# Performance work log

Hardware: AMD Instinct MI355X
Metric: run time of the kernel (lower is better)

The kernel has to match this reference:

```python
import jax, jax.numpy as jnp
import numpy as np

B, T, D = 2, 2048, 2048
H, KV = 16, 4
HD = D // H  # 128
ROPE_BASE = 10000.0


def _rope(t):
    # t: [B, h, T, HD]; faithful to torch apply_rope (even/odd split, concat halves)
    pos = jnp.arange(T, dtype=t.dtype)
    inv_freq = 1.0 / (ROPE_BASE ** (jnp.arange(0, HD, 2, dtype=t.dtype) / HD))
    ang = jnp.einsum('t,f->tf', pos, inv_freq)  # [T, HD/2]
    sin = jnp.sin(ang)[None, None]
    cos = jnp.cos(ang)[None, None]
    t1, t2 = t[..., ::2], t[..., 1::2]
    return jnp.concatenate([t1 * cos - t2 * sin, t1 * sin + t2 * cos], axis=-1)


def setup_inputs() -> dict:
    key = jax.random.key(0)
    kx, kq, kk, kv, ko = jax.random.split(key, 5)
    x = jax.random.normal(kx, (B, T, D), dtype=jnp.float32)
    s = 0.02
    Wq = jax.random.normal(kq, (D, D), dtype=jnp.float32) * s
    Wk = jax.random.normal(kk, (D, KV * HD), dtype=jnp.float32) * s
    Wv = jax.random.normal(kv, (D, KV * HD), dtype=jnp.float32) * s
    Wo = jax.random.normal(ko, (D, D), dtype=jnp.float32) * s
    return {"x": x, "Wq": Wq, "Wk": Wk, "Wv": Wv, "Wo": Wo}


def reference(x, Wq, Wk, Wv, Wo):
    # projections (nn.Linear, no bias)
    q = (x @ Wq).reshape(B, T, H, HD).transpose(0, 2, 1, 3)    # [B,H,T,HD]
    k = (x @ Wk).reshape(B, T, KV, HD).transpose(0, 2, 1, 3)   # [B,KV,T,HD]
    v = (x @ Wv).reshape(B, T, KV, HD).transpose(0, 2, 1, 3)
    q = _rope(q)
    k = _rope(k)
    # GQA: repeat_interleave kv heads to full head count
    g = H // KV
    k = jnp.repeat(k, g, axis=1)
    v = jnp.repeat(v, g, axis=1)
    # causal SDPA, default scale 1/sqrt(head_dim)
    scale = 1.0 / jnp.sqrt(jnp.array(HD, dtype=x.dtype))
    scores = jnp.einsum('bhqd,bhkd->bhqk', q, k) * scale
    mask = jnp.tril(jnp.ones((T, T), dtype=bool))
    scores = jnp.where(mask, scores, jnp.finfo(scores.dtype).min)
    attn = jax.nn.softmax(scores, axis=-1)
    out = jnp.einsum('bhqk,bhkd->bhqd', attn, v)               # [B,H,T,HD]
    out = out.transpose(0, 2, 1, 3).reshape(B, T, D)
    return out @ Wo
```

## Files before the change

### kernel.cpp

```cpp
#include <hip/hip_runtime.h>
#include <math.h>

#define BB 2
#define TT 2048
#define DD 2048
#define HH 16
#define KVHN 4
#define HDIM 128
#define NKV 3072

typedef unsigned short u16;
typedef unsigned int u32;
typedef __bf16 bf16x8 __attribute__((ext_vector_type(8)));
typedef float  f32x4  __attribute__((ext_vector_type(4)));

#define AS1 __attribute__((address_space(1)))
#define AS3 __attribute__((address_space(3)))

__device__ __forceinline__ void dma16(const u16* g, u16* l) {
  __builtin_amdgcn_global_load_lds((const AS1 u32*)g, (AS3 u32*)l, 16, 0, 0);
}

__device__ __forceinline__ u16 f2bf(float f) {
  u32 u = __float_as_uint(f);
  u32 r = (u + 0x7FFFu + ((u >> 16) & 1u)) >> 16;
  return (u16)r;
}
__device__ __forceinline__ float bf2f(u32 h) { return __uint_as_float(h << 16); }

__device__ __forceinline__ u32 pack2(float a, float b) {
  union { __bf16 h[2]; u32 u; } cv;
  cv.h[0] = (__bf16)a; cv.h[1] = (__bf16)b;
  return cv.u;
}

__global__ __launch_bounds__(256) void castf2b(const float* __restrict__ in,
                                               u16* __restrict__ out) {
  size_t i4 = (size_t)blockIdx.x * 256 + threadIdx.x;
  float4 v = *(const float4*)(in + i4 * 4);
  ushort4 o;
  o.x = f2bf(v.x); o.y = f2bf(v.y); o.z = f2bf(v.z); o.w = f2bf(v.w);
  *(ushort4*)(out + i4 * 4) = o;
}

__global__ __launch_bounds__(256) void tcast(const float* __restrict__ W,
                                             u16* __restrict__ WT,
                                             int K, int N) {
  __shared__ float tile[32][33];
  const int n0 = blockIdx.x * 32, k0 = blockIdx.y * 32;
  const int r = threadIdx.x >> 3;
  const int c4 = (threadIdx.x & 7) * 4;
  float4 v = *(const float4*)(W + (size_t)(k0 + r) * N + n0 + c4);
  tile[r][c4 + 0] = v.x; tile[r][c4 + 1] = v.y;
  tile[r][c4 + 2] = v.z; tile[r][c4 + 3] = v.w;
  __syncthreads();
  ushort4 o;
  o.x = f2bf(tile[c4 + 0][r]); o.y = f2bf(tile[c4 + 1][r]);
  o.z = f2bf(tile[c4 + 2][r]); o.w = f2bf(tile[c4 + 3][r]);
  *(ushort4*)(WT + (size_t)(n0 + r) * K + k0 + c4) = o;
}

template <int OUT_BF16>
__global__ __launch_bounds__(256) void gemm2(const u16* __restrict__ A,
                                             const u16* __restrict__ BT,
                                             void* __restrict__ Cv,
                                             int N, int K) {
  __shared__ u16 As[128 * 32];
  __shared__ u16 Bs[128 * 32];
  const int t = threadIdx.x;
  const int l = t & 63, w = t >> 6;
  const int lm = l & 15, quad = l >> 4;
  const int wm = w & 1, wn = w >> 1;
  const int m0 = blockIdx.y * 128, n0 = blockIdx.x * 128;
  const int wu = __builtin_amdgcn_readfirstlane(w);

  f32x4 acc[4][4];
  #pragma unroll
  for (int i = 0; i < 4; ++i)
    #pragma unroll
    for (int j = 0; j < 4; ++j) acc[i][j] = (f32x4){0.f, 0.f, 0.f, 0.f};

  for (int k0 = 0; k0 < K; k0 += 32) {
    __syncthreads();
    #pragma unroll
    for (int i = 0; i < 2; ++i) {
      int p0 = (wu * 2 + i) * 64;
      int p = p0 + l;
      int row = p >> 2, c = p & 3;
      dma16(A  + (size_t)(m0 + row) * K + k0 + c * 8, &As[p0 * 8]);
      dma16(BT + (size_t)(n0 + row) * K + k0 + c * 8, &Bs[p0 * 8]);
    }
    __syncthreads();
    bf16x8 a[4], bq[4];
    #pragma unroll
    for (int i = 0; i < 4; ++i)
      a[i] = *(const bf16x8*)&As[(wm * 64 + i * 16 + lm) * 32 + quad * 8];
    #pragma unroll
    for (int j = 0; j < 4; ++j)
      bq[j] = *(const bf16x8*)&Bs[(wn * 64 + j * 16 + lm) * 32 + quad * 8];
    #pragma unroll
    for (int i = 0; i < 4; ++i)
      #pragma unroll
      for (int j = 0; j < 4; ++j)
        acc[i][j] = __builtin_amdgcn_mfma_f32_16x16x32_bf16(a[i], bq[j], acc[i][j], 0, 0, 0);
  }

  #pragma unroll
  for (int i = 0; i < 4; ++i) {
    #pragma unroll
    for (int r = 0; r < 4; ++r) {
      size_t gr = (size_t)(m0 + wm * 64 + i * 16 + quad * 4 + r);
      #pragma unroll
      for (int j = 0; j < 4; ++j) {
        int gc = n0 + wn * 64 + j * 16 + lm;
        if (OUT_BF16) ((u16*)Cv)[gr * N + gc] = f2bf(acc[i][j][r]);
        else          ((float*)Cv)[gr * N + gc] = acc[i][j][r];
      }
    }
  }
}

__global__ __launch_bounds__(256) void rope2(u16* p) {
  const int row = blockIdx.x;
  const int pos = row & (TT - 1);
  u16* base = p + (size_t)row * NKV;
  float e0[5], e1[5];
  #pragma unroll
  for (int i = 0; i < 5; ++i) {
    int item = threadIdx.x + i * 256;
    int h20 = item >> 6, f = item & 63;
    int col = (h20 < 16) ? h20 * 128 : 2048 + (h20 - 16) * 128;
    u32 u = *(const u32*)(base + col + 2 * f);
    e0[i] = bf2f(u & 0xffffu);
    e1[i] = bf2f(u >> 16);
  }
  __syncthreads();
  #pragma unroll
  for (int i = 0; i < 5; ++i) {
    int item = threadIdx.x + i * 256;
    int h20 = item >> 6, f = item & 63;
    int col = (h20 < 16) ? h20 * 128 : 2048 + (h20 - 16) * 128;
    float sc = (h20 < 16) ? 0.08838834764831845f : 1.0f;
    float inv = exp2f((float)f * -0.20762050593046898f);
    float ang = (float)pos * inv;
    float sn = sinf(ang), cs = cosf(ang);
    base[col + f]      = f2bf((e0[i] * cs - e1[i] * sn) * sc);
    base[col + 64 + f] = f2bf((e0[i] * sn + e1[i] * cs) * sc);
  }
}

__global__ __launch_bounds__(256) void vtrans(const u16* __restrict__ QKV,
                                              u16* __restrict__ Vt) {
  __shared__ u16 tl[64][72];
  const int t0 = blockIdx.x * 64;
  const int y  = blockIdx.y;
  const int b  = blockIdx.z;
  #pragma unroll
  for (int i = 0; i < 2; ++i) {
    int idx = threadIdx.x + i * 256;
    int r = idx >> 3, c = (idx & 7) * 8;
    *(uint4*)&tl[r][c] =
        *(const uint4*)(QKV + (size_t)(b * TT + t0 + r) * NKV + 2560 + y * 64 + c);
  }
  __syncthreads();
  const int vh = y >> 1;
  #pragma unroll
  for (int i = 0; i < 2; ++i) {
    int idx = threadIdx.x + i * 256;
    int dr = idx >> 3, tc = (idx & 7) * 8;
    u16 tmp[8];
    #pragma unroll
    for (int j = 0; j < 8; ++j) tmp[j] = tl[tc + j][dr];
    int dloc = (y & 1) * 64 + dr;
    *(uint4*)(Vt + (size_t)((b * KVHN + vh) * HDIM + dloc) * TT + t0 + tc) =
        *(const uint4*)tmp;
  }
}

__global__ __launch_bounds__(256, 2) void attn2(const u16* __restrict__ QKV,
                                                const u16* __restrict__ Vt,
                                                u16* __restrict__ Ob) {
  __shared__ u16 KsA[64 * 128], KsB[64 * 128];
  __shared__ u16 VsA[128 * 64], VsB[128 * 64];
  __shared__ u16 Pw[4 * 2048];
  const int t = threadIdx.x;
  const int l = t & 63, w = t >> 6;
  const int lm = l & 15, quad = l >> 4;
  const int px = blockIdx.x, h = blockIdx.y, b = blockIdx.z;
  const int kvh = h >> 2;
  const int qlo = px * 64, qhi = (31 - px) * 64;
  const int last = 31 - px;
  const int wu = __builtin_amdgcn_readfirstlane(w);
  u16* pwv = &Pw[w * 2048];
  constexpr float L2E = 1.4426950408889634f;

  bf16x8 qf[2][4];
  {
    size_t r0 = (size_t)(b * TT + qlo + w * 16 + lm) * NKV + h * HDIM;
    size_t r1 = (size_t)(b * TT + qhi + w * 16 + lm) * NKV + h * HDIM;
    #pragma unroll
    for (int ks = 0; ks < 4; ++ks) {
      qf[0][ks] = *(const bf16x8*)(QKV + r0 + ks * 32 + quad * 8);
      qf[1][ks] = *(const bf16x8*)(QKV + r1 + ks * 32 + quad * 8);
    }
  }

  f32x4 o[8][2];
  #pragma unroll
  for (int i = 0; i < 8; ++i)
    #pragma unroll
    for (int n = 0; n < 2; ++n) o[i][n] = (f32x4){0.f, 0.f, 0.f, 0.f};
  float m_[2] = {-1e30f, -1e30f}, l_[2] = {0.f, 0.f};

  auto stageK = [&](int kt, u16* dst) {
    #pragma unroll
    for (int i = 0; i < 4; ++i) {
      int p0 = (wu * 4 + i) * 64;
      int p = p0 + l;
      int row = p >> 4, cp = p & 15, cl = cp ^ (row & 15);
      dma16(QKV + (size_t)(b * TT + kt * 64 + row) * NKV + 2048 + kvh * HDIM + cl * 8,
            dst + p0 * 8);
    }
  };
  auto stageV = [&](int kt, u16* dst) {
    #pragma unroll
    for (int i = 0; i < 4; ++i) {
      int p0 = (wu * 4 + i) * 64;
      int p = p0 + l;
      int d = p >> 3, cp = p & 7, cl = cp ^ (d & 7);
      dma16(Vt + (size_t)((b * KVHN + kvh) * HDIM + d) * TT + kt * 64 + cl * 8,
            dst + p0 * 8);
    }
  };

  auto body = [&](int kt, u16* kcur, u16* vcur, u16* knext, u16* vnext) {
    __syncthreads();
    const bool pf = kt < last;
    if (pf) stageV(kt + 1, vnext);
    const bool lo = (kt <= px);

    f32x4 s[4][2];
    #pragma unroll
    for (int mt = 0; mt < 4; ++mt) {
      s[mt][0] = (f32x4){0.f, 0.f, 0.f, 0.f};
      s[mt][1] = (f32x4){0.f, 0.f, 0.f, 0.f};
    }
    #pragma unroll
    for (int ks = 0; ks < 4; ++ks) {
      #pragma unroll
      for (int mt = 0; mt < 4; ++mt) {
        bf16x8 kb = *(const bf16x8*)&kcur[(mt * 16 + lm) * 128 + (((ks * 4 + quad) ^ lm) * 8)];
        if (lo) s[mt][0] = __builtin_amdgcn_mfma_f32_16x16x32_bf16(kb, qf[0][ks], s[mt][0], 0, 0, 0);
        s[mt][1] = __builtin_amdgcn_mfma_f32_16x16x32_bf16(kb, qf[1][ks], s[mt][1], 0, 0, 0);
      }
    }
    if (pf) stageK(kt + 1, knext);

    if (kt == px) {
      #pragma unroll
      for (int mt = 0; mt < 4; ++mt)
        #pragma unroll
        for (int r = 0; r < 4; ++r) {
          int kv = kt * 64 + mt * 16 + quad * 4 + r;
          if (kv > qlo + w * 16 + lm) s[mt][0][r] = -1e30f;
        }
    }
    if (kt == last) {
      #pragma unroll
      for (int mt = 0; mt < 4; ++mt)
        #pragma unroll
        for (int r = 0; r < 4; ++r) {
          int kv = kt * 64 + mt * 16 + quad * 4 + r;
          if (kv > qhi + w * 16 + lm) s[mt][1][r] = -1e30f;
        }
    }

    float al[2] = {1.f, 1.f};
    #pragma unroll
    for (int nt = 0; nt < 2; ++nt) {
      if (nt == 0 && !lo) continue;
      float mx = -1e30f;
      #pragma unroll
      for (int mt = 0; mt < 4; ++mt)
        #pragma unroll
        for (int r = 0; r < 4; ++r) mx = fmaxf(mx, s[mt][nt][r]);
      mx = fmaxf(mx, __shfl_xor(mx, 16));
      mx = fmaxf(mx, __shfl_xor(mx, 32));
      float mn = fmaxf(m_[nt], mx);
      al[nt] = exp2f((m_[nt] - mn) * L2E);
      m_[nt] = mn;
      float sum = 0.f;
      #pragma unroll
      for (int mt = 0; mt < 4; ++mt)
        #pragma unroll
        for (int r = 0; r < 4; ++r) {
          float pv = exp2f((s[mt][nt][r] - mn) * L2E);
          s[mt][nt][r] = pv;
          sum += pv;
        }
      sum += __shfl_xor(sum, 16);
      sum += __shfl_xor(sum, 32);
      l_[nt] = l_[nt] * al[nt] + sum;

      #pragma unroll
      for (int mt = 0; mt < 4; ++mt) {
        u32 p01 = pack2(s[mt][nt][0], s[mt][nt][1]);
        u32 p23 = pack2(s[mt][nt][2], s[mt][nt][3]);
        int phys = (mt * 2 + (quad >> 1)) ^ (lm & 7);
        int addr = (nt * 16 + lm) * 64 + phys * 8 + (quad & 1) * 4;
        uint2 uv; uv.x = p01; uv.y = p23;
        *(uint2*)&pwv[addr] = uv;
      }
      if (__any(al[nt] < 1.0f)) {
        #pragma unroll
        for (int mt2 = 0; mt2 < 8; ++mt2)
          #pragma unroll
          for (int r = 0; r < 4; ++r) o[mt2][nt][r] *= al[nt];
      }
    }

    #pragma unroll
    for (int ks2 = 0; ks2 < 2; ++ks2) {
      int coff = ((ks2 * 4 + quad) ^ (lm & 7)) * 8;
      bf16x8 pb0, pb1;
      if (lo) pb0 = *(const bf16x8*)&pwv[lm * 64 + coff];
      pb1 = *(const bf16x8*)&pwv[(16 + lm) * 64 + coff];
      #pragma unroll
      for (int mt2 = 0; mt2 < 8; ++mt2) {
        bf16x8 vb = *(const bf16x8*)&vcur[(mt2 * 16 + lm) * 64 + coff];
        if (lo) o[mt2][0] = __builtin_amdgcn_mfma_f32_16x16x32_bf16(vb, pb0, o[mt2][0], 0, 0, 0);
        o[mt2][1] = __builtin_amdgcn_mfma_f32_16x16x32_bf16(vb, pb1, o[mt2][1], 0, 0, 0);
      }
    }
  };

  stageK(0, KsA); stageV(0, VsA);
  for (int kt = 0; kt <= last; ++kt) {
    if ((kt & 1) == 0) body(kt, KsA, VsA, KsB, VsB);
    else               body(kt, KsB, VsB, KsA, VsA);
  }

  #pragma unroll
  for (int nt = 0; nt < 2; ++nt) {
    float inv = 1.f / l_[nt];
    #pragma unroll
    for (int mt2 = 0; mt2 < 8; ++mt2) {
      u32 a0 = pack2(o[mt2][nt][0] * inv, o[mt2][nt][1] * inv);
      u32 a1 = pack2(o[mt2][nt][2] * inv, o[mt2][nt][3] * inv);
      int phys = (mt2 * 2 + (quad >> 1)) ^ (lm & 7);
      int addr = lm * 128 + phys * 8 + (quad & 1) * 4;
      uint2 uv; uv.x = a0; uv.y = a1;
      *(uint2*)&pwv[addr] = uv;
    }
    int qt0 = nt ? qhi : qlo;
    #pragma unroll
    for (int i = 0; i < 4; ++i) {
      int p = i * 64 + l;
      int row = p >> 4, cl = p & 15;
      int cph = cl ^ (row & 7);
      uint4 val = *(const uint4*)&pwv[row * 128 + cph * 8];
      *(uint4*)(Ob + (size_t)(b * TT + qt0 + w * 16 + row) * DD + h * HDIM + cl * 8) = val;
    }
  }
}

extern "C" void kernel_launch(void* const* d_in, const int* in_sizes, int n_in,
                              void* d_out, int out_size, void* d_ws, size_t ws_size,
                              hipStream_t stream) {
  const float* x  = (const float*)d_in[0];
  const float* Wq = (const float*)d_in[1];
  const float* Wk = (const float*)d_in[2];
  const float* Wv = (const float*)d_in[3];
  const float* Wo = (const float*)d_in[4];
  float* out = (float*)d_out;

  u16* xb    = (u16*)d_ws;
  u16* WqkvT = xb + 8388608;
  u16* WoT   = xb + 14680064;
  u16* Vt    = WqkvT;
  u16* Ob    = xb;
  u16* QKVb  = (u16*)d_out;

  dim3 blk(256);
  castf2b<<<8192, blk, 0, stream>>>(x, xb);
  tcast<<<dim3(64, 64), blk, 0, stream>>>(Wq, WqkvT, DD, DD);
  tcast<<<dim3(16, 64), blk, 0, stream>>>(Wk, WqkvT + (size_t)2048 * DD, DD, 512);
  tcast<<<dim3(16, 64), blk, 0, stream>>>(Wv, WqkvT + (size_t)2560 * DD, DD, 512);
  tcast<<<dim3(64, 64), blk, 0, stream>>>(Wo, WoT, DD, DD);

  gemm2<1><<<dim3(NKV / 128, 32), blk, 0, stream>>>(xb, WqkvT, QKVb, NKV, DD);
  rope2<<<BB * TT, blk, 0, stream>>>(QKVb);
  vtrans<<<dim3(32, 8, BB), blk, 0, stream>>>(QKVb, Vt);
  attn2<<<dim3(16, HH, BB), blk, 0, stream>>>(QKVb, Vt, Ob);
  gemm2<0><<<dim3(DD / 128, 32), blk, 0, stream>>>(Ob, WoT, out, DD, DD);
}
```

Measured before the change: 341.5 us.

## Merge prep and rope/vtrans launches; simplify attention to one q-tile per block

Four cast/transpose kernels become a single block-indexed prep launch, and the rope and V-transpose kernels become one launch, which removes launch gaps. The attention kernel drops the paired lo/hi query tiles and the double-buffered K/V staging. Each block now handles one 64-row query tile with single-buffered LDS, and heaviest tiles are scheduled first. Launch bounds are raised to 4 blocks per CU. This trades explicit prefetch overlap for higher occupancy and lower register and LDS use, relying on other resident blocks to hide load latency.

```diff
diff --git a/kernel.cpp b/kernel.cpp
--- a/kernel.cpp
+++ b/kernel.cpp
@@ -34,22 +34,12 @@
   return cv.u;
 }
 
-__global__ __launch_bounds__(256) void castf2b(const float* __restrict__ in,
-                                               u16* __restrict__ out) {
-  size_t i4 = (size_t)blockIdx.x * 256 + threadIdx.x;
-  float4 v = *(const float4*)(in + i4 * 4);
-  ushort4 o;
-  o.x = f2bf(v.x); o.y = f2bf(v.y); o.z = f2bf(v.z); o.w = f2bf(v.w);
-  *(ushort4*)(out + i4 * 4) = o;
-}
-
-__global__ __launch_bounds__(256) void tcast(const float* __restrict__ W,
-                                             u16* __restrict__ WT,
-                                             int K, int N) {
-  __shared__ float tile[32][33];
-  const int n0 = blockIdx.x * 32, k0 = blockIdx.y * 32;
-  const int r = threadIdx.x >> 3;
-  const int c4 = (threadIdx.x & 7) * 4;
+__device__ __forceinline__ void tc_body(const float* __restrict__ W,
+                                        u16* __restrict__ WT,
+                                        int N, int n0, int k0, int tid,
+                                        float (*tile)[33]) {
+  const int r = tid >> 3;
+  const int c4 = (tid & 7) * 4;
   float4 v = *(const float4*)(W + (size_t)(k0 + r) * N + n0 + c4);
   tile[r][c4 + 0] = v.x; tile[r][c4 + 1] = v.y;
   tile[r][c4 + 2] = v.z; tile[r][c4 + 3] = v.w;
@@ -57,7 +47,39 @@
   ushort4 o;
   o.x = f2bf(tile[c4 + 0][r]); o.y = f2bf(tile[c4 + 1][r]);
   o.z = f2bf(tile[c4 + 2][r]); o.w = f2bf(tile[c4 + 3][r]);
-  *(ushort4*)(WT + (size_t)(n0 + r) * K + k0 + c4) = o;
+  *(ushort4*)(WT + (size_t)(n0 + r) * DD + k0 + c4) = o;
+}
+
+__global__ __launch_bounds__(256) void prep(const float* __restrict__ x,
+                                            const float* __restrict__ Wq,
+                                            const float* __restrict__ Wk,
+                                            const float* __restrict__ Wv,
+                                            const float* __restrict__ Wo,
+                                            u16* __restrict__ xb,
+                                            u16* __restrict__ WqkvT,
+                                            u16* __restrict__ WoT) {
+  __shared__ float tile[32][33];
+  const int bid = blockIdx.x;
+  const int tid = threadIdx.x;
+  if (bid < 8192) {
+    size_t i4 = (size_t)bid * 256 + tid;
+    float4 v = *(const float4*)(x + i4 * 4);
+    ushort4 o;
+    o.x = f2bf(v.x); o.y = f2bf(v.y); o.z = f2bf(v.z); o.w = f2bf(v.w);
+    *(ushort4*)(xb + i4 * 4) = o;
+  } else if (bid < 12288) {
+    int idx = bid - 8192;
+    tc_body(Wq, WqkvT, DD, (idx & 63) * 32, (idx >> 6) * 32, tid, tile);
+  } else if (bid < 13312) {
+    int idx = bid - 12288;
+    tc_body(Wk, WqkvT + (size_t)2048 * DD, 512, (idx & 15) * 32, (idx >> 4) * 32, tid, tile);
+  } else if (bid < 14336) {
+    int idx = bid - 13312;
+    tc_body(Wv, WqkvT + (size_t)2560 * DD, 512, (idx & 15) * 32, (idx >> 4) * 32, tid, tile);
+  } else {
+    int idx = bid - 14336;
+    tc_body(Wo, WoT, DD, (idx & 63) * 32, (idx >> 6) * 32, tid, tile);
+  }
 }
 
 template <int OUT_BF16>
@@ -120,246 +142,207 @@
   }
 }
 
-__global__ __launch_bounds__(256) void rope2(u16* p) {
-  const int row = blockIdx.x;
-  const int pos = row & (TT - 1);
-  u16* base = p + (size_t)row * NKV;
-  float e0[5], e1[5];
-  #pragma unroll
-  for (int i = 0; i < 5; ++i) {
-    int item = threadIdx.x + i * 256;
-    int h20 = item >> 6, f = item & 63;
-    int col = (h20 < 16) ? h20 * 128 : 2048 + (h20 - 16) * 128;
-    u32 u = *(const u32*)(base + col + 2 * f);
-    e0[i] = bf2f(u & 0xffffu);
-    e1[i] = bf2f(u >> 16);
-  }
-  __syncthreads();
-  #pragma unroll
-  for (int i = 0; i < 5; ++i) {
-    int item = threadIdx.x + i * 256;
-    int h20 = item >> 6, f = item & 63;
-    int col = (h20 < 16) ? h20 * 128 : 2048 + (h20 - 16) * 128;
-    float sc = (h20 < 16) ? 0.08838834764831845f : 1.0f;
-    float inv = exp2f((float)f * -0.20762050593046898f);
-    float ang = (float)pos * inv;
-    float sn = sinf(ang), cs = cosf(ang);
-    base[col + f]      = f2bf((e0[i] * cs - e1[i] * sn) * sc);
-    base[col + 64 + f] = f2bf((e0[i] * sn + e1[i] * cs) * sc);
-  }
-}
-
-__global__ __launch_bounds__(256) void vtrans(const u16* __restrict__ QKV,
+__global__ __launch_bounds__(256) void ropevt(u16* __restrict__ QKV,
                                               u16* __restrict__ Vt) {
   __shared__ u16 tl[64][72];
-  const int t0 = blockIdx.x * 64;
-  const int y  = blockIdx.y;
-  const int b  = blockIdx.z;
-  #pragma unroll
-  for (int i = 0; i < 2; ++i) {
-    int idx = threadIdx.x + i * 256;
-    int r = idx >> 3, c = (idx & 7) * 8;
-    *(uint4*)&tl[r][c] =
-        *(const uint4*)(QKV + (size_t)(b * TT + t0 + r) * NKV + 2560 + y * 64 + c);
-  }
-  __syncthreads();
-  const int vh = y >> 1;
-  #pragma unroll
-  for (int i = 0; i < 2; ++i) {
-    int idx = threadIdx.x + i * 256;
-    int dr = idx >> 3, tc = (idx & 7) * 8;
-    u16 tmp[8];
-    #pragma unroll
-    for (int j = 0; j < 8; ++j) tmp[j] = tl[tc + j][dr];
-    int dloc = (y & 1) * 64 + dr;
-    *(uint4*)(Vt + (size_t)((b * KVHN + vh) * HDIM + dloc) * TT + t0 + tc) =
-        *(const uint4*)tmp;
-  }
-}
-
-__global__ __launch_bounds__(256, 2) void attn2(const u16* __restrict__ QKV,
+  const int bid = blockIdx.x;
+  if (bid < 4096) {
+    const int row = bid;
+    const int pos = row & (TT - 1);
+    u16* base = QKV + (size_t)row * NKV;
+    float e0[5], e1[5];
+    #pragma unroll
+    for (int i = 0; i < 5; ++i) {
+      int item = threadIdx.x + i * 256;
+      int h20 = item >> 6, f = item & 63;
+      int col = (h20 < 16) ? h20 * 128 : 2048 + (h20 - 16) * 128;
+      u32 u = *(const u32*)(base + col + 2 * f);
+      e0[i] = bf2f(u & 0xffffu);
+      e1[i] = bf2f(u >> 16);
+    }
+    __syncthreads();
+    #pragma unroll
+    for (int i = 0; i < 5; ++i) {
+      int item = threadIdx.x + i * 256;
+      int h20 = item >> 6, f = item & 63;
+      int col = (h20 < 16) ? h20 * 128 : 2048 + (h20 - 16) * 128;
+      float sc = (h20 < 16) ? 0.08838834764831845f : 1.0f;
+      float inv = exp2f((float)f * -0.20762050593046898f);
+      float ang = (float)pos * inv;
+      float sn = sinf(ang), cs = cosf(ang);
+      base[col + f]      = f2bf((e0[i] * cs - e1[i] * sn) * sc);
+      base[col + 64 + f] = f2bf((e0[i] * sn + e1[i] * cs) * sc);
+    }
+  } else {
+    const int v = bid - 4096;
+    const int t0 = (v & 31) * 64;
+    const int y  = (v >> 5) & 7;
+    const int b  = v >> 8;
+    #pragma unroll
+    for (int i = 0; i < 2; ++i) {
+      int idx = threadIdx.x + i * 256;
+      int r = idx >> 3, c = (idx & 7) * 8;
+      *(uint4*)&tl[r][c] =
+          *(const uint4*)(QKV + (size_t)(b * TT + t0 + r) * NKV + 2560 + y * 64 + c);
+    }
+    __syncthreads();
+    const int vh = y >> 1;
+    #pragma unroll
+    for (int i = 0; i < 2; ++i) {
+      int idx = threadIdx.x + i * 256;
+      int dr = idx >> 3, tc = (idx & 7) * 8;
+      u16 tmp[8];
+      #pragma unroll
+      for (int j = 0; j < 8; ++j) tmp[j] = tl[tc + j][dr];
+      int dloc = (y & 1) * 64 + dr;
+      *(uint4*)(Vt + (size_t)((b * KVHN + vh) * HDIM + dloc) * TT + t0 + tc) =
+          *(const uint4*)tmp;
+    }
+  }
+}
+
+__global__ __launch_bounds__(256, 4) void attn3(const u16* __restrict__ QKV,
                                                 const u16* __restrict__ Vt,
                                                 u16* __restrict__ Ob) {
-  __shared__ u16 KsA[64 * 128], KsB[64 * 128];
-  __shared__ u16 VsA[128 * 64], VsB[128 * 64];
-  __shared__ u16 Pw[4 * 2048];
+  __shared__ u16 Ks[64 * 128];
+  __shared__ u16 Vs[128 * 64];
+  __shared__ u16 Pw[4 * 1024];
   const int t = threadIdx.x;
   const int l = t & 63, w = t >> 6;
   const int lm = l & 15, quad = l >> 4;
-  const int px = blockIdx.x, h = blockIdx.y, b = blockIdx.z;
+  const int qt = 31 - (int)blockIdx.x;
+  const int h = blockIdx.y, b = blockIdx.z;
   const int kvh = h >> 2;
-  const int qlo = px * 64, qhi = (31 - px) * 64;
-  const int last = 31 - px;
   const int wu = __builtin_amdgcn_readfirstlane(w);
-  u16* pwv = &Pw[w * 2048];
+  u16* pwv = &Pw[w * 1024];
   constexpr float L2E = 1.4426950408889634f;
 
-  bf16x8 qf[2][4];
+  bf16x8 qf[4];
   {
-    size_t r0 = (size_t)(b * TT + qlo + w * 16 + lm) * NKV + h * HDIM;
-    size_t r1 = (size_t)(b * TT + qhi + w * 16 + lm) * NKV + h * HDIM;
-    #pragma unroll
-    for (int ks = 0; ks < 4; ++ks) {
-      qf[0][ks] = *(const bf16x8*)(QKV + r0 + ks * 32 + quad * 8);
-      qf[1][ks] = *(const bf16x8*)(QKV + r1 + ks * 32 + quad * 8);
-    }
-  }
-
-  f32x4 o[8][2];
+    size_t r0 = (size_t)(b * TT + qt * 64 + w * 16 + lm) * NKV + h * HDIM;
+    #pragma unroll
+    for (int ks = 0; ks < 4; ++ks)
+      qf[ks] = *(const bf16x8*)(QKV + r0 + ks * 32 + quad * 8);
+  }
+
+  f32x4 o[8];
   #pragma unroll
-  for (int i = 0; i < 8; ++i)
-    #pragma unroll
-    for (int n = 0; n < 2; ++n) o[i][n] = (f32x4){0.f, 0.f, 0.f, 0.f};
-  float m_[2] = {-1e30f, -1e30f}, l_[2] = {0.f, 0.f};
-
-  auto stageK = [&](int kt, u16* dst) {
+  for (int i = 0; i < 8; ++i) o[i] = (f32x4){0.f, 0.f, 0.f, 0.f};
+  float m_ = -1e30f, l_ = 0.f;
+
+  for (int kt = 0; kt <= qt; ++kt) {
     #pragma unroll
     for (int i = 0; i < 4; ++i) {
       int p0 = (wu * 4 + i) * 64;
       int p = p0 + l;
       int row = p >> 4, cp = p & 15, cl = cp ^ (row & 15);
       dma16(QKV + (size_t)(b * TT + kt * 64 + row) * NKV + 2048 + kvh * HDIM + cl * 8,
-            dst + p0 * 8);
-    }
-  };
-  auto stageV = [&](int kt, u16* dst) {
+            &Ks[p0 * 8]);
+    }
     #pragma unroll
     for (int i = 0; i < 4; ++i) {
       int p0 = (wu * 4 + i) * 64;
       int p = p0 + l;
       int d = p >> 3, cp = p & 7, cl = cp ^ (d & 7);
       dma16(Vt + (size_t)((b * KVHN + kvh) * HDIM + d) * TT + kt * 64 + cl * 8,
-            dst + p0 * 8);
-    }
-  };
-
-  auto body = [&](int kt, u16* kcur, u16* vcur, u16* knext, u16* vnext) {
-    __syncthreads();
-    const bool pf = kt < last;
-    if (pf) stageV(kt + 1, vnext);
-    const bool lo = (kt <= px);
-
-    f32x4 s[4][2];
-    #pragma unroll
-    for (int mt = 0; mt < 4; ++mt) {
-      s[mt][0] = (f32x4){0.f, 0.f, 0.f, 0.f};
-      s[mt][1] = (f32x4){0.f, 0.f, 0.f, 0.f};
-    }
-    #pragma unroll
-    for (int ks = 0; ks < 4; ++ks) {
+            &Vs[p0 * 8]);
+    }
+    __syncthreads();
+
+    f32x4 s[4];
+    #pragma unroll
+    for (int mt = 0; mt < 4; ++mt) s[mt] = (f32x4){0.f, 0.f, 0.f, 0.f};
+    #pragma unroll
+    for (int ks = 0; ks < 4; ++ks)
       #pragma unroll
       for (int mt = 0; mt < 4; ++mt) {
-        bf16x8 kb = *(const bf16x8*)&kcur[(mt * 16 + lm) * 128 + (((ks * 4 + quad) ^ lm) * 8)];
-        if (lo) s[mt][0] = __builtin_amdgcn_mfma_f32_16x16x32_bf16(kb, qf[0][ks], s[mt][0], 0, 0, 0);
-        s[mt][1] = __builtin_amdgcn_mfma_f32_16x16x32_bf16(kb, qf[1][ks], s[mt][1], 0, 0, 0);
+        bf16x8 kb = *(const bf16x8*)&Ks[(mt * 16 + lm) * 128 + (((ks * 4 + quad) ^ lm) * 8)];
+        s[mt] = __builtin_amdgcn_mfma_f32_16x16x32_bf16(kb, qf[ks], s[mt], 0, 0, 0);
       }
-    }
-    if (pf) stageK(kt + 1, knext);
-
-    if (kt == px) {
+
+    if (kt == qt) {
       #pragma unroll
       for (int mt = 0; mt < 4; ++mt)
         #pragma unroll
         for (int r = 0; r < 4; ++r) {
           int kv = kt * 64 + mt * 16 + quad * 4 + r;
-          if (kv > qlo + w * 16 + lm) s[mt][0][r] = -1e30f;
+          if (kv > qt * 64 + w * 16 + lm) s[mt][r] = -1e30f;
         }
     }
-    if (kt == last) {
-      #pragma unroll
-      for (int mt = 0; mt < 4; ++mt)
+
+    float mx = -1e30f;
+    #pragma unroll
+    for (int mt = 0; mt < 4; ++mt)
+      #pragma unroll
+      for (int r = 0; r < 4; ++r) mx = fmaxf(mx, s[mt][r]);
+    mx = fmaxf(mx, __shfl_xor(mx, 16));
+    mx = fmaxf(mx, __shfl_xor(mx, 32));
+    float mn = fmaxf(m_, mx);
+    float al = exp2f((m_ - mn) * L2E);
+    m_ = mn;
+    float sum = 0.f;
+    #pragma unroll
+    for (int mt = 0; mt < 4; ++mt)
+      #pragma unroll
+      for (int r = 0; r < 4; ++r) {
+        float pv = exp2f((s[mt][r] - mn) * L2E);
+        s[mt][r] = pv;
+        sum += pv;
+      }
+    sum += __shfl_xor(sum, 16);
+    sum += __shfl_xor(sum, 32);
+    l_ = l_ * al + sum;
+
+    #pragma unroll
+    for (int mt = 0; mt < 4; ++mt) {
+      u32 p01 = pack2(s[mt][0], s[mt][1]);
+      u32 p23 = pack2(s[mt][2], s[mt][3]);
+      int phys = (mt * 2 + (quad >> 1)) ^ (lm & 7);
+      int addr = lm * 64 + phys * 8 + (quad & 1) * 4;
+      uint2 uv; uv.x = p01; uv.y = p23;
+      *(uint2*)&pwv[addr] = uv;
+    }
+    if (__any(al < 1.0f)) {
+      #pragma unroll
+      for (int mt2 = 0; mt2 < 8; ++mt2)
         #pragma unroll
-        for (int r = 0; r < 4; ++r) {
-          int kv = kt * 64 + mt * 16 + quad * 4 + r;
-          if (kv > qhi + w * 16 + lm) s[mt][1][r] = -1e30f;
-        }
-    }
-
-    float al[2] = {1.f, 1.f};
-    #pragma unroll
-    for (int nt = 0; nt < 2; ++nt) {
-      if (nt == 0 && !lo) continue;
-      float mx = -1e30f;
-      #pragma unroll
-      for (int mt = 0; mt < 4; ++mt)
-        #pragma unroll
-        for (int r = 0; r < 4; ++r) mx = fmaxf(mx, s[mt][nt][r]);
-      mx = fmaxf(mx, __shfl_xor(mx, 16));
-      mx = fmaxf(mx, __shfl_xor(mx, 32));
-      float mn = fmaxf(m_[nt], mx);
-      al[nt] = exp2f((m_[nt] - mn) * L2E);
-      m_[nt] = mn;
-      float sum = 0.f;
-      #pragma unroll
-      for (int mt = 0; mt < 4; ++mt)
-        #pragma unroll
-        for (int r = 0; r < 4; ++r) {
-          float pv = exp2f((s[mt][nt][r] - mn) * L2E);
-          s[mt][nt][r] = pv;
-          sum += pv;
-        }
-      sum += __shfl_xor(sum, 16);
-      sum += __shfl_xor(sum, 32);
-      l_[nt] = l_[nt] * al[nt] + sum;
-
-      #pragma unroll
-      for (int mt = 0; mt < 4; ++mt) {
-        u32 p01 = pack2(s[mt][nt][0], s[mt][nt][1]);
-        u32 p23 = pack2(s[mt][nt][2], s[mt][nt][3]);
-        int phys = (mt * 2 + (quad >> 1)) ^ (lm & 7);
-        int addr = (nt * 16 + lm) * 64 + phys * 8 + (quad & 1) * 4;
-        uint2 uv; uv.x = p01; uv.y = p23;
-        *(uint2*)&pwv[addr] = uv;
-      }
-      if (__any(al[nt] < 1.0f)) {
-        #pragma unroll
-        for (int mt2 = 0; mt2 < 8; ++mt2)
-          #pragma unroll
-          for (int r = 0; r < 4; ++r) o[mt2][nt][r] *= al[nt];
-      }
+        for (int r = 0; r < 4; ++r) o[mt2][r] *= al;
     }
 
     #pragma unroll
     for (int ks2 = 0; ks2 < 2; ++ks2) {
       int coff = ((ks2 * 4 + quad) ^ (lm & 7)) * 8;
-      bf16x8 pb0, pb1;
-      if (lo) pb0 = *(const bf16x8*)&pwv[lm * 64 + coff];
-      pb1 = *(const bf16x8*)&pwv[(16 + lm) * 64 + coff];
+      bf16x8 pb = *(const bf16x8*)&pwv[lm * 64 + coff];
       #pragma unroll
       for (int mt2 = 0; mt2 < 8; ++mt2) {
-        bf16x8 vb = *(const bf16x8*)&vcur[(mt2 * 16 + lm) * 64 + coff];
-        if (lo) o[mt2][0] = __builtin_amdgcn_mfma_f32_16x16x32_bf16(vb, pb0, o[mt2][0], 0, 0, 0);
-        o[mt2][1] = __builtin_amdgcn_mfma_f32_16x16x32_bf16(vb, pb1, o[mt2][1], 0, 0, 0);
+        bf16x8 vb = *(const bf16x8*)&Vs[(mt2 * 16 + lm) * 64 + coff];
+        o[mt2] = __builtin_amdgcn_mfma_f32_16x16x32_bf16(vb, pb, o[mt2], 0, 0, 0);
       }
     }
-  };
-
-  stageK(0, KsA); stageV(0, VsA);
-  for (int kt = 0; kt <= last; ++kt) {
-    if ((kt & 1) == 0) body(kt, KsA, VsA, KsB, VsB);
-    else               body(kt, KsB, VsB, KsA, VsA);
-  }
-
+    __syncthreads();
+  }
+
+  float inv = 1.f / l_;
   #pragma unroll
-  for (int nt = 0; nt < 2; ++nt) {
-    float inv = 1.f / l_[nt];
-    #pragma unroll
-    for (int mt2 = 0; mt2 < 8; ++mt2) {
-      u32 a0 = pack2(o[mt2][nt][0] * inv, o[mt2][nt][1] * inv);
-      u32 a1 = pack2(o[mt2][nt][2] * inv, o[mt2][nt][3] * inv);
-      int phys = (mt2 * 2 + (quad >> 1)) ^ (lm & 7);
-      int addr = lm * 128 + phys * 8 + (quad & 1) * 4;
+  for (int half = 0; half < 2; ++half) {
+    #pragma unroll
+    for (int m2 = 0; m2 < 4; ++m2) {
+      int mt2 = half * 4 + m2;
+      u32 a0 = pack2(o[mt2][0] * inv, o[mt2][1] * inv);
+      u32 a1 = pack2(o[mt2][2] * inv, o[mt2][3] * inv);
+      int phys = (m2 * 2 + (quad >> 1)) ^ (lm & 7);
+      int addr = lm * 64 + phys * 8 + (quad & 1) * 4;
       uint2 uv; uv.x = a0; uv.y = a1;
       *(uint2*)&pwv[addr] = uv;
     }
-    int qt0 = nt ? qhi : qlo;
-    #pragma unroll
-    for (int i = 0; i < 4; ++i) {
+    #pragma unroll
+    for (int i = 0; i < 2; ++i) {
       int p = i * 64 + l;
-      int row = p >> 4, cl = p & 15;
+      int row = p >> 3, cl = p & 7;
       int cph = cl ^ (row & 7);
-      uint4 val = *(const uint4*)&pwv[row * 128 + cph * 8];
-      *(uint4*)(Ob + (size_t)(b * TT + qt0 + w * 16 + row) * DD + h * HDIM + cl * 8) = val;
+      uint4 val = *(const uint4*)&pwv[row * 64 + cph * 8];
+      *(uint4*)(Ob + (size_t)(b * TT + qt * 64 + w * 16 + row) * DD +
+                h * HDIM + half * 64 + cl * 8) = val;
     }
   }
 }
@@ -382,15 +365,9 @@
   u16* QKVb  = (u16*)d_out;
 
   dim3 blk(256);
-  castf2b<<<8192, blk, 0, stream>>>(x, xb);
-  tcast<<<dim3(64, 64), blk, 0, stream>>>(Wq, WqkvT, DD, DD);
-  tcast<<<dim3(16, 64), blk, 0, stream>>>(Wk, WqkvT + (size_t)2048 * DD, DD, 512);
-  tcast<<<dim3(16, 64), blk, 0, stream>>>(Wv, WqkvT + (size_t)2560 * DD, DD, 512);
-  tcast<<<dim3(64, 64), blk, 0, stream>>>(Wo, WoT, DD, DD);
-
+  prep<<<18432, blk, 0, stream>>>(x, Wq, Wk, Wv, Wo, xb, WqkvT, WoT);
   gemm2<1><<<dim3(NKV / 128, 32), blk, 0, stream>>>(xb, WqkvT, QKVb, NKV, DD);
-  rope2<<<BB * TT, blk, 0, stream>>>(QKVb);
-  vtrans<<<dim3(32, 8, BB), blk, 0, stream>>>(QKVb, Vt);
-  attn2<<<dim3(16, HH, BB), blk, 0, stream>>>(QKVb, Vt, Ob);
+  ropevt<<<4608, blk, 0, stream>>>(QKVb, Vt);
+  attn3<<<dim3(32, HH, BB), blk, 0, stream>>>(QKVb, Vt, Ob);
   gemm2<0><<<dim3(DD / 128, 32), blk, 0, stream>>>(Ob, WoT, out, DD, DD);
 }
```

Result: slower. 353.4 us (+3.5%).

## Fuse RoPE and V transpose into QKV GEMM epilogue, merge prep kernels

Applied to the files above, without the earlier changes.

The five cast/transpose launches are merged into one prep kernel with block-range dispatch. The QKV GEMM epilogue now applies RoPE and the q scale in registers, pairing even and odd columns with a lane shuffle. For the V tiles it writes a transposed V through swizzled shared memory, which removes the separate rope and vtrans kernels and their global round trips. V now lives in the output buffer past the QKV region. The cost is a heavier epilogue that computes sincos per element and uses extra syncs.

```diff
diff --git a/kernel.cpp b/kernel.cpp
--- a/kernel.cpp
+++ b/kernel.cpp
@@ -34,22 +34,12 @@
   return cv.u;
 }
 
-__global__ __launch_bounds__(256) void castf2b(const float* __restrict__ in,
-                                               u16* __restrict__ out) {
-  size_t i4 = (size_t)blockIdx.x * 256 + threadIdx.x;
-  float4 v = *(const float4*)(in + i4 * 4);
-  ushort4 o;
-  o.x = f2bf(v.x); o.y = f2bf(v.y); o.z = f2bf(v.z); o.w = f2bf(v.w);
-  *(ushort4*)(out + i4 * 4) = o;
-}
-
-__global__ __launch_bounds__(256) void tcast(const float* __restrict__ W,
-                                             u16* __restrict__ WT,
-                                             int K, int N) {
-  __shared__ float tile[32][33];
-  const int n0 = blockIdx.x * 32, k0 = blockIdx.y * 32;
-  const int r = threadIdx.x >> 3;
-  const int c4 = (threadIdx.x & 7) * 4;
+__device__ __forceinline__ void tc_body(const float* __restrict__ W,
+                                        u16* __restrict__ WT,
+                                        int N, int n0, int k0, int tid,
+                                        float (*tile)[33]) {
+  const int r = tid >> 3;
+  const int c4 = (tid & 7) * 4;
   float4 v = *(const float4*)(W + (size_t)(k0 + r) * N + n0 + c4);
   tile[r][c4 + 0] = v.x; tile[r][c4 + 1] = v.y;
   tile[r][c4 + 2] = v.z; tile[r][c4 + 3] = v.w;
@@ -57,13 +47,151 @@
   ushort4 o;
   o.x = f2bf(tile[c4 + 0][r]); o.y = f2bf(tile[c4 + 1][r]);
   o.z = f2bf(tile[c4 + 2][r]); o.w = f2bf(tile[c4 + 3][r]);
-  *(ushort4*)(WT + (size_t)(n0 + r) * K + k0 + c4) = o;
-}
-
-template <int OUT_BF16>
+  *(ushort4*)(WT + (size_t)(n0 + r) * DD + k0 + c4) = o;
+}
+
+__global__ __launch_bounds__(256) void prep(const float* __restrict__ x,
+                                            const float* __restrict__ Wq,
+                                            const float* __restrict__ Wk,
+                                            const float* __restrict__ Wv,
+                                            const float* __restrict__ Wo,
+                                            u16* __restrict__ xb,
+                                            u16* __restrict__ WqkvT,
+                                            u16* __restrict__ WoT) {
+  __shared__ float tile[32][33];
+  const int bid = blockIdx.x;
+  const int tid = threadIdx.x;
+  if (bid < 8192) {
+    size_t i4 = (size_t)bid * 256 + tid;
+    float4 v = *(const float4*)(x + i4 * 4);
+    ushort4 o;
+    o.x = f2bf(v.x); o.y = f2bf(v.y); o.z = f2bf(v.z); o.w = f2bf(v.w);
+    *(ushort4*)(xb + i4 * 4) = o;
+  } else if (bid < 12288) {
+    int idx = bid - 8192;
+    tc_body(Wq, WqkvT, DD, (idx & 63) * 32, (idx >> 6) * 32, tid, tile);
+  } else if (bid < 13312) {
+    int idx = bid - 12288;
+    tc_body(Wk, WqkvT + (size_t)2048 * DD, 512, (idx & 15) * 32, (idx >> 4) * 32, tid, tile);
+  } else if (bid < 14336) {
+    int idx = bid - 13312;
+    tc_body(Wv, WqkvT + (size_t)2560 * DD, 512, (idx & 15) * 32, (idx >> 4) * 32, tid, tile);
+  } else {
+    int idx = bid - 14336;
+    tc_body(Wo, WoT, DD, (idx & 63) * 32, (idx >> 6) * 32, tid, tile);
+  }
+}
+
+__global__ __launch_bounds__(256) void gemm_qkv(const u16* __restrict__ A,
+                                                const u16* __restrict__ BT,
+                                                u16* __restrict__ QKV,
+                                                u16* __restrict__ Vt) {
+  __shared__ u16 smem[128 * 64];
+  u16* As = smem;
+  u16* Bs = smem + 128 * 32;
+  const int t = threadIdx.x;
+  const int l = t & 63, w = t >> 6;
+  const int lm = l & 15, quad = l >> 4;
+  const int wm = w & 1, wn = w >> 1;
+  const int tile = blockIdx.x;
+  const int m0 = blockIdx.y * 128, n0 = tile * 128;
+  const int wu = __builtin_amdgcn_readfirstlane(w);
+
+  f32x4 acc[4][4];
+  #pragma unroll
+  for (int i = 0; i < 4; ++i)
+    #pragma unroll
+    for (int j = 0; j < 4; ++j) acc[i][j] = (f32x4){0.f, 0.f, 0.f, 0.f};
+
+  for (int k0 = 0; k0 < DD; k0 += 32) {
+    __syncthreads();
+    #pragma unroll
+    for (int i = 0; i < 2; ++i) {
+      int p0 = (wu * 2 + i) * 64;
+      int p = p0 + l;
+      int row = p >> 2, c = p & 3;
+      dma16(A  + (size_t)(m0 + row) * DD + k0 + c * 8, &As[p0 * 8]);
+      dma16(BT + (size_t)(n0 + row) * DD + k0 + c * 8, &Bs[p0 * 8]);
+    }
+    __syncthreads();
+    bf16x8 a[4], bq[4];
+    #pragma unroll
+    for (int i = 0; i < 4; ++i)
+      a[i] = *(const bf16x8*)&As[(wm * 64 + i * 16 + lm) * 32 + quad * 8];
+    #pragma unroll
+    for (int j = 0; j < 4; ++j)
+      bq[j] = *(const bf16x8*)&Bs[(wn * 64 + j * 16 + lm) * 32 + quad * 8];
+    #pragma unroll
+    for (int i = 0; i < 4; ++i)
+      #pragma unroll
+      for (int j = 0; j < 4; ++j)
+        acc[i][j] = __builtin_amdgcn_mfma_f32_16x16x32_bf16(a[i], bq[j], acc[i][j], 0, 0, 0);
+  }
+
+  const int b = m0 >> 11;
+  const int t0 = m0 & 2047;
+  if (tile < 20) {
+    const float sc = (tile < 16) ? 0.08838834764831845f : 1.0f;
+    const int odd = lm & 1;
+    #pragma unroll
+    for (int j = 0; j < 4; ++j) {
+      int cl = wn * 64 + j * 16 + lm;
+      int f = cl >> 1;
+      float wf = exp2f((float)f * -0.20762050593046898f);
+      size_t gc = n0 + (odd ? 64 + f : f);
+      #pragma unroll
+      for (int i = 0; i < 4; ++i) {
+        #pragma unroll
+        for (int r = 0; r < 4; ++r) {
+          int row = wm * 64 + i * 16 + quad * 4 + r;
+          float own = acc[i][j][r];
+          float oth = __shfl_xor(own, 1);
+          float e = odd ? oth : own;
+          float o = odd ? own : oth;
+          float ang = (float)(t0 + row) * wf;
+          float sn, cs;
+          __sincosf(ang, &sn, &cs);
+          float res = odd ? (e * sn + o * cs) : (e * cs - o * sn);
+          QKV[(size_t)(m0 + row) * NKV + gc] = f2bf(res * sc);
+        }
+      }
+    }
+  } else {
+    const int vh = tile - 20;
+    #pragma unroll
+    for (int half = 0; half < 2; ++half) {
+      __syncthreads();
+      if (wm == half) {
+        #pragma unroll
+        for (int j = 0; j < 4; ++j) {
+          int d = wn * 64 + j * 16 + lm;
+          #pragma unroll
+          for (int i = 0; i < 4; ++i)
+            #pragma unroll
+            for (int r = 0; r < 4; ++r) {
+              int tl = i * 16 + quad * 4 + r;
+              int pt = tl ^ ((d & 7) * 8);
+              smem[d * 64 + pt] = f2bf(acc[i][j][r]);
+            }
+        }
+      }
+      __syncthreads();
+      #pragma unroll
+      for (int it = 0; it < 4; ++it) {
+        int p = it * 256 + t;
+        int d = p >> 3, c = p & 7;
+        int pc = c ^ (d & 7);
+        uint4 val = *(const uint4*)&smem[d * 64 + pc * 8];
+        *(uint4*)(Vt + ((size_t)((b * KVHN + vh) * HDIM + d)) * TT +
+                  t0 + half * 64 + c * 8) = val;
+      }
+    }
+  }
+}
+
 __global__ __launch_bounds__(256) void gemm2(const u16* __restrict__ A,
                                              const u16* __restrict__ BT,
-                                             void* __restrict__ Cv,
+                                             float* __restrict__ Cv,
                                              int N, int K) {
   __shared__ u16 As[128 * 32];
   __shared__ u16 Bs[128 * 32];
@@ -113,67 +241,9 @@
       #pragma unroll
       for (int j = 0; j < 4; ++j) {
         int gc = n0 + wn * 64 + j * 16 + lm;
-        if (OUT_BF16) ((u16*)Cv)[gr * N + gc] = f2bf(acc[i][j][r]);
-        else          ((float*)Cv)[gr * N + gc] = acc[i][j][r];
-      }
-    }
-  }
-}
-
-__global__ __launch_bounds__(256) void rope2(u16* p) {
-  const int row = blockIdx.x;
-  const int pos = row & (TT - 1);
-  u16* base = p + (size_t)row * NKV;
-  float e0[5], e1[5];
-  #pragma unroll
-  for (int i = 0; i < 5; ++i) {
-    int item = threadIdx.x + i * 256;
-    int h20 = item >> 6, f = item & 63;
-    int col = (h20 < 16) ? h20 * 128 : 2048 + (h20 - 16) * 128;
-    u32 u = *(const u32*)(base + col + 2 * f);
-    e0[i] = bf2f(u & 0xffffu);
-    e1[i] = bf2f(u >> 16);
-  }
-  __syncthreads();
-  #pragma unroll
-  for (int i = 0; i < 5; ++i) {
-    int item = threadIdx.x + i * 256;
-    int h20 = item >> 6, f = item & 63;
-    int col = (h20 < 16) ? h20 * 128 : 2048 + (h20 - 16) * 128;
-    float sc = (h20 < 16) ? 0.08838834764831845f : 1.0f;
-    float inv = exp2f((float)f * -0.20762050593046898f);
-    float ang = (float)pos * inv;
-    float sn = sinf(ang), cs = cosf(ang);
-    base[col + f]      = f2bf((e0[i] * cs - e1[i] * sn) * sc);
-    base[col + 64 + f] = f2bf((e0[i] * sn + e1[i] * cs) * sc);
-  }
-}
-
-__global__ __launch_bounds__(256) void vtrans(const u16* __restrict__ QKV,
-                                              u16* __restrict__ Vt) {
-  __shared__ u16 tl[64][72];
-  const int t0 = blockIdx.x * 64;
-  const int y  = blockIdx.y;
-  const int b  = blockIdx.z;
-  #pragma unroll
-  for (int i = 0; i < 2; ++i) {
-    int idx = threadIdx.x + i * 256;
-    int r = idx >> 3, c = (idx & 7) * 8;
-    *(uint4*)&tl[r][c] =
-        *(const uint4*)(QKV + (size_t)(b * TT + t0 + r) * NKV + 2560 + y * 64 + c);
-  }
-  __syncthreads();
-  const int vh = y >> 1;
-  #pragma unroll
-  for (int i = 0; i < 2; ++i) {
-    int idx = threadIdx.x + i * 256;
-    int dr = idx >> 3, tc = (idx & 7) * 8;
-    u16 tmp[8];
-    #pragma unroll
-    for (int j = 0; j < 8; ++j) tmp[j] = tl[tc + j][dr];
-    int dloc = (y & 1) * 64 + dr;
-    *(uint4*)(Vt + (size_t)((b * KVHN + vh) * HDIM + dloc) * TT + t0 + tc) =
-        *(const uint4*)tmp;
+        Cv[gr * N + gc] = acc[i][j][r];
+      }
+    }
   }
 }
 
@@ -377,20 +447,13 @@
   u16* xb    = (u16*)d_ws;
   u16* WqkvT = xb + 8388608;
   u16* WoT   = xb + 14680064;
-  u16* Vt    = WqkvT;
   u16* Ob    = xb;
   u16* QKVb  = (u16*)d_out;
+  u16* Vt    = QKVb + (size_t)4096 * NKV;
 
   dim3 blk(256);
-  castf2b<<<8192, blk, 0, stream>>>(x, xb);
-  tcast<<<dim3(64, 64), blk, 0, stream>>>(Wq, WqkvT, DD, DD);
-  tcast<<<dim3(16, 64), blk, 0, stream>>>(Wk, WqkvT + (size_t)2048 * DD, DD, 512);
-  tcast<<<dim3(16, 64), blk, 0, stream>>>(Wv, WqkvT + (size_t)2560 * DD, DD, 512);
-  tcast<<<dim3(64, 64), blk, 0, stream>>>(Wo, WoT, DD, DD);
-
-  gemm2<1><<<dim3(NKV / 128, 32), blk, 0, stream>>>(xb, WqkvT, QKVb, NKV, DD);
-  rope2<<<BB * TT, blk, 0, stream>>>(QKVb);
-  vtrans<<<dim3(32, 8, BB), blk, 0, stream>>>(QKVb, Vt);
+  prep<<<18432, blk, 0, stream>>>(x, Wq, Wk, Wv, Wo, xb, WqkvT, WoT);
+  gemm_qkv<<<dim3(NKV / 128, 32), blk, 0, stream>>>(xb, WqkvT, QKVb, Vt);
   attn2<<<dim3(16, HH, BB), blk, 0, stream>>>(QKVb, Vt, Ob);
-  gemm2<0><<<dim3(DD / 128, 32), blk, 0, stream>>>(Ob, WoT, out, DD, DD);
-}
+  gemm2<<<dim3(DD / 128, 32), blk, 0, stream>>>(Ob, WoT, out, DD, DD);
+}
```

Result: slower. 368.3 us (+7.9%).
